# Kernel tuning notes

Measured on AMD Instinct MI355X. Metric: run time of the kernel, lower is better.

## Reference

```python
import jax, jax.numpy as jnp
import numpy as np

EPS = 1e-7

def sphere_log(p, q):
    # Riemannian log on unit sphere; p, q broadcastable, points along last axis.
    dot = jnp.clip(jnp.sum(p * q, axis=-1, keepdims=True), -1.0 + EPS, 1.0 - EPS)
    theta = jnp.arccos(dot)
    v = q - dot * p                      # tangent direction (unnormalized)
    nv = jnp.linalg.norm(v, axis=-1, keepdims=True)
    nv_safe = jnp.where(nv < EPS, 1.0, nv)
    factor = jnp.where(nv < EPS, 1.0, theta / nv_safe)  # theta/||v|| -> 1 as q->p
    return factor * v

def sphere_exp(p, v):
    # Riemannian exp on unit sphere.
    n = jnp.linalg.norm(v, axis=-1, keepdims=True)
    n_safe = jnp.where(n < EPS, 1.0, n)
    s = jnp.where(n < EPS, 1.0, jnp.sin(n_safe) / n_safe)  # sinc(||v||)
    return jnp.cos(n) * p + s * v

def setup_inputs() -> dict:
    key = jax.random.key(0)
    k1, k2 = jax.random.split(key)
    B, L, C_in, C_out, d = 4, 256, 64, 64, 64
    x = jax.random.normal(k1, (B, L, C_in, d), dtype=jnp.float32)
    x = x / jnp.linalg.norm(x, axis=-1, keepdims=True)  # points on S^{d-1}
    # param 'w': truncated_normal(stddev=1) with shape (n_in, n_out)
    w_raw = jax.random.truncated_normal(k2, -2.0, 2.0, (C_in, C_out), dtype=jnp.float32)
    return {"x": x, "w_raw": w_raw}

def reference(x, w_raw):
    B, L, C_in, d = x.shape
    C_out = w_raw.shape[1]
    # softmax-like positive, column-normalized weights
    w = jnp.exp(w_raw - np.log(C_in).astype(np.float32))
    w = w / w.sum(axis=0)[None]          # (C_in, C_out)

    xr = x.reshape(B * L, C_in, d)       # (N, C_in, d)
    # init at first in-channel point, broadcast over out channels: (N, C_out, d)
    a = jnp.broadcast_to(xr[:, 0][:, None, :], (B * L, C_out, d))

    # 3-step fixed-point iteration toward weighted Frechet mean (scan unroll=3)
    for _ in range(3):
        logs = sphere_log(a[:, :, None, :], xr[:, None, :, :])  # (N, C_out, C_in, d)
        grad = jnp.einsum('io,noid->nod', w, logs)              # (N, C_out, d)
        a = sphere_exp(a, grad)

    return a.reshape(B, L, C_out, d)
```

## Files before the change

### kernel.cpp

```cpp
#include <hip/hip_runtime.h>

#define EPSF 1e-7f
#define TS2 72

typedef __bf16 bf16;
typedef __attribute__((ext_vector_type(8))) __bf16 bf16x8;
typedef __attribute__((ext_vector_type(4))) __bf16 bf16x4;
typedef __attribute__((ext_vector_type(4))) float f32x4;
typedef __attribute__((ext_vector_type(2))) float f32x2;

__device__ __forceinline__ float quad_sum(float v) {
  v += __shfl_xor(v, 16, 64);
  v += __shfl_xor(v, 32, 64);
  return v;
}

__global__ __launch_bounds__(256, 4) void mfd_fc_mfma(
    const float* __restrict__ x, const float* __restrict__ wraw,
    float* __restrict__ out) {
  __shared__ __align__(16) bf16 Xrow[64 * TS2];
  __shared__ __align__(16) bf16 Xt[64 * TS2];
  __shared__ __align__(16) bf16 AC[64 * TS2];

  const int n = blockIdx.x;
  const int tid = threadIdx.x;
  const int wv = tid >> 6;
  const int lane = tid & 63;
  const int ln15 = lane & 15;
  const int quad = lane >> 4;
  const int q4 = 4 * quad;
  const int olane = 16 * wv + ln15;
  const float* xn = x + (size_t)n * 4096;

  const f32x2 ONE2 = {1.0f, 1.0f};
  const f32x2 PC3 = {-0.0187292994f, -0.0187292994f};
  const f32x2 PC2 = {0.0742610070f, 0.0742610070f};
  const f32x2 PC1 = {-0.2121144013f, -0.2121144013f};
  const f32x2 PC0 = {1.5707288f, 1.5707288f};
  const f32x2 PI2 = {3.14159265358979f, 3.14159265358979f};

#pragma unroll
  for (int t = 0; t < 4; ++t) {
    int idx = tid + t * 256;
    int i = idx >> 4;
    int c4 = (idx & 15) << 2;
    float4 v = reinterpret_cast<const float4*>(xn)[idx];
    bf16x4 b;
    b[0] = (bf16)v.x; b[1] = (bf16)v.y; b[2] = (bf16)v.z; b[3] = (bf16)v.w;
    *reinterpret_cast<bf16x4*>(&Xrow[i * TS2 + c4]) = b;
  }

  f32x2 wfp[4][2];
  {
    f32x2 cs2 = {0.f, 0.f};
#pragma unroll
    for (int t = 0; t < 4; ++t)
#pragma unroll
      for (int h = 0; h < 2; ++h) {
        f32x2 e;
        e.x = __expf(wraw[(16 * t + q4 + 2 * h) * 64 + olane]);
        e.y = __expf(wraw[(16 * t + q4 + 2 * h + 1) * 64 + olane]);
        wfp[t][h] = e;
        cs2 = cs2 + e;
      }
    float inv = __builtin_amdgcn_rcpf(quad_sum(cs2.x + cs2.y));
    f32x2 inv2 = {inv, inv};
#pragma unroll
    for (int t = 0; t < 4; ++t)
#pragma unroll
      for (int h = 0; h < 2; ++h) wfp[t][h] = wfp[t][h] * inv2;
  }

  float a_reg[4][4];
#pragma unroll
  for (int t = 0; t < 4; ++t) {
    float4 v = *reinterpret_cast<const float4*>(&xn[16 * t + q4]);
    a_reg[t][0] = v.x; a_reg[t][1] = v.y; a_reg[t][2] = v.z; a_reg[t][3] = v.w;
  }

  __syncthreads();

  bf16x8 xrf[4][2];
#pragma unroll
  for (int t = 0; t < 4; ++t)
#pragma unroll
    for (int ks = 0; ks < 2; ++ks)
      xrf[t][ks] = *reinterpret_cast<const bf16x8*>(
          &Xrow[(16 * t + ln15) * TS2 + ks * 32 + quad * 8]);

  bf16x8 x0f[2];
#pragma unroll
  for (int ks = 0; ks < 2; ++ks)
    x0f[ks] = *reinterpret_cast<const bf16x8*>(&Xrow[ks * 32 + quad * 8]);

  {
    int dd = tid & 63, ih = tid >> 6;
    bf16 tmp[16];
#pragma unroll
    for (int j = 0; j < 16; ++j) tmp[j] = Xrow[(16 * ih + j) * TS2 + dd];
    *reinterpret_cast<bf16x8*>(&Xt[dd * TS2 + 16 * ih]) =
        *reinterpret_cast<bf16x8*>(&tmp[0]);
    *reinterpret_cast<bf16x8*>(&Xt[dd * TS2 + 16 * ih + 8]) =
        *reinterpret_cast<bf16x8*>(&tmp[8]);
  }

  bf16* acrow = &AC[olane * TS2];
  f32x2* a2 = reinterpret_cast<f32x2*>(&a_reg[0][0]);

#pragma unroll
  for (int it = 0; it < 3; ++it) {
    f32x4 acc[4] = {f32x4{0,0,0,0}, f32x4{0,0,0,0}, f32x4{0,0,0,0}, f32x4{0,0,0,0}};
#pragma unroll
    for (int ks = 0; ks < 2; ++ks) {
      bf16x8 bfA = (it == 0)
          ? x0f[ks]
          : *reinterpret_cast<const bf16x8*>(&acrow[ks * 32 + quad * 8]);
#pragma unroll
      for (int t = 0; t < 4; ++t)
        acc[t] = __builtin_amdgcn_mfma_f32_16x16x32_bf16(xrf[t][ks], bfA, acc[t], 0, 0, 0);
    }

#pragma unroll
    for (int t = 0; t < 4; ++t) {
      bf16x4 cpk;
#pragma unroll
      for (int h = 0; h < 2; ++h) {
        f32x2 d2;
        d2.x = __builtin_amdgcn_fmed3f(acc[t][2 * h],     -1.0f + EPSF, 1.0f - EPSF);
        d2.y = __builtin_amdgcn_fmed3f(acc[t][2 * h + 1], -1.0f + EPSF, 1.0f - EPSF);
        f32x2 nd = -d2;
        f32x2 ax; ax.x = fmaxf(d2.x, nd.x); ax.y = fmaxf(d2.y, nd.y);
        f32x2 p1 = ONE2 + ax;
        f32x2 m1 = ONE2 - ax;
        f32x2 q2, r2;
        q2.x = __builtin_amdgcn_rsqf(p1.x); q2.y = __builtin_amdgcn_rsqf(p1.y);
        r2.x = __builtin_amdgcn_rsqf(m1.x); r2.y = __builtin_amdgcn_rsqf(m1.y);
        f32x2 pa = PC3 * ax + PC2;
        pa = pa * ax + PC1;
        pa = pa * ax + PC0;
        f32x2 nb = PI2 * r2 - pa;
        f32x2 sel;
        sel.x = (d2.x < 0.f) ? nb.x : pa.x;
        sel.y = (d2.y < 0.f) ? nb.y : pa.y;
        f32x2 cf = (sel * q2) * wfp[t][h];
        cpk[2 * h]     = (bf16)cf.x;
        cpk[2 * h + 1] = (bf16)cf.y;
      }
      *reinterpret_cast<bf16x4*>(&acrow[16 * t + q4]) = cpk;
    }

    if (it == 0) __syncthreads();

    f32x4 g[4] = {f32x4{0,0,0,0}, f32x4{0,0,0,0}, f32x4{0,0,0,0}, f32x4{0,0,0,0}};
#pragma unroll
    for (int ks = 0; ks < 2; ++ks) {
      bf16x8 cf = *reinterpret_cast<const bf16x8*>(&acrow[ks * 32 + quad * 8]);
#pragma unroll
      for (int t = 0; t < 4; ++t) {
        bf16x8 xtf = *reinterpret_cast<const bf16x8*>(
            &Xt[(16 * t + ln15) * TS2 + ks * 32 + quad * 8]);
        g[t] = __builtin_amdgcn_mfma_f32_16x16x32_bf16(xtf, cf, g[t], 0, 0, 0);
      }
    }

    f32x2* g2 = reinterpret_cast<f32x2*>(&g[0]);
    f32x2 sdp = {0.f, 0.f}, ggp = {0.f, 0.f};
#pragma unroll
    for (int u = 0; u < 8; ++u) {
      sdp = a2[u] * g2[u] + sdp;
      ggp = g2[u] * g2[u] + ggp;
    }
    float sdv = quad_sum(sdp.x + sdp.y);
    float gg  = quad_sum(ggp.x + ggp.y);
    float gn2 = fmaxf(gg - sdv * sdv, 0.f);
    float nrm = __builtin_amdgcn_sqrtf(gn2);
    float rev = nrm * 0.15915494309189535f;
    float sn_ = __builtin_amdgcn_sinf(rev);
    float cn  = __builtin_amdgcn_cosf(rev);
    float sn = (nrm < EPSF) ? 1.0f : sn_ * __builtin_amdgcn_rcpf(nrm);
    float coefA = cn - sn * sdv;
    f32x2 cA2 = {coefA, coefA}, sn2 = {sn, sn};
#pragma unroll
    for (int u = 0; u < 8; ++u)
      a2[u] = cA2 * a2[u] + sn2 * g2[u];
    if (it < 2) {
#pragma unroll
      for (int t = 0; t < 4; ++t) {
        bf16x4 apk;
#pragma unroll
        for (int r = 0; r < 4; ++r) apk[r] = (bf16)a_reg[t][r];
        *reinterpret_cast<bf16x4*>(&acrow[16 * t + q4]) = apk;
      }
    }
  }

  float* outn = out + (size_t)n * 4096;
#pragma unroll
  for (int t = 0; t < 4; ++t) {
    float4 v4;
    v4.x = a_reg[t][0]; v4.y = a_reg[t][1];
    v4.z = a_reg[t][2]; v4.w = a_reg[t][3];
    *reinterpret_cast<float4*>(&outn[olane * 64 + 16 * t + q4]) = v4;
  }
}

extern "C" void kernel_launch(void* const* d_in, const int* in_sizes, int n_in,
                              void* d_out, int out_size, void* d_ws, size_t ws_size,
                              hipStream_t stream) {
  const float* x = (const float*)d_in[0];
  const float* wraw = (const float*)d_in[1];
  float* out = (float*)d_out;
  (void)d_ws; (void)ws_size;

  int N = in_sizes[0] / 4096;
  mfd_fc_mfma<<<N, 256, 0, stream>>>(x, wraw, out);
}
```

Baseline: 77.70 us.

## Process two samples per block to amortize weight setup and add ILP

Each block now handles two independent points (N/2 blocks), interleaving their MFMA chains and elementwise stages so the two samples' dependent work can overlap. The weight softmax load and normalization are computed once per two samples. LDS per block doubles and register use rises, so launch bounds drop from 4 to 2 blocks per CU, which lowers occupancy. The N/2 grid assumes N is even.

```diff
diff --git a/kernel.cpp b/kernel.cpp
--- a/kernel.cpp
+++ b/kernel.cpp
@@ -2,6 +2,7 @@
 
 #define EPSF 1e-7f
 #define TS2 72
+#define SLDS (64 * TS2)
 
 typedef __bf16 bf16;
 typedef __attribute__((ext_vector_type(8))) __bf16 bf16x8;
@@ -15,14 +16,13 @@
   return v;
 }
 
-__global__ __launch_bounds__(256, 4) void mfd_fc_mfma(
+__global__ __launch_bounds__(256, 2) void mfd_fc_mfma(
     const float* __restrict__ x, const float* __restrict__ wraw,
     float* __restrict__ out) {
-  __shared__ __align__(16) bf16 Xrow[64 * TS2];
-  __shared__ __align__(16) bf16 Xt[64 * TS2];
-  __shared__ __align__(16) bf16 AC[64 * TS2];
-
-  const int n = blockIdx.x;
+  __shared__ __align__(16) bf16 Xrow[2 * SLDS];
+  __shared__ __align__(16) bf16 Xt[2 * SLDS];
+  __shared__ __align__(16) bf16 AC[2 * SLDS];
+
   const int tid = threadIdx.x;
   const int wv = tid >> 6;
   const int lane = tid & 63;
@@ -30,7 +30,7 @@
   const int quad = lane >> 4;
   const int q4 = 4 * quad;
   const int olane = 16 * wv + ln15;
-  const float* xn = x + (size_t)n * 4096;
+  const float* xb = x + (size_t)blockIdx.x * 8192;
 
   const f32x2 ONE2 = {1.0f, 1.0f};
   const f32x2 PC3 = {-0.0187292994f, -0.0187292994f};
@@ -40,14 +40,19 @@
   const f32x2 PI2 = {3.14159265358979f, 3.14159265358979f};
 
 #pragma unroll
-  for (int t = 0; t < 4; ++t) {
-    int idx = tid + t * 256;
-    int i = idx >> 4;
-    int c4 = (idx & 15) << 2;
-    float4 v = reinterpret_cast<const float4*>(xn)[idx];
-    bf16x4 b;
-    b[0] = (bf16)v.x; b[1] = (bf16)v.y; b[2] = (bf16)v.z; b[3] = (bf16)v.w;
-    *reinterpret_cast<bf16x4*>(&Xrow[i * TS2 + c4]) = b;
+  for (int s = 0; s < 2; ++s) {
+    const float* xn = xb + s * 4096;
+    bf16* XR = Xrow + s * SLDS;
+#pragma unroll
+    for (int t = 0; t < 4; ++t) {
+      int idx = tid + t * 256;
+      int i = idx >> 4;
+      int c4 = (idx & 15) << 2;
+      float4 v = reinterpret_cast<const float4*>(xn)[idx];
+      bf16x4 b;
+      b[0] = (bf16)v.x; b[1] = (bf16)v.y; b[2] = (bf16)v.z; b[3] = (bf16)v.w;
+      *reinterpret_cast<bf16x4*>(&XR[i * TS2 + c4]) = b;
+    }
   }
 
   f32x2 wfp[4][2];
@@ -71,137 +76,168 @@
       for (int h = 0; h < 2; ++h) wfp[t][h] = wfp[t][h] * inv2;
   }
 
-  float a_reg[4][4];
-#pragma unroll
-  for (int t = 0; t < 4; ++t) {
-    float4 v = *reinterpret_cast<const float4*>(&xn[16 * t + q4]);
-    a_reg[t][0] = v.x; a_reg[t][1] = v.y; a_reg[t][2] = v.z; a_reg[t][3] = v.w;
-  }
+  float a_reg[2][4][4];
+#pragma unroll
+  for (int s = 0; s < 2; ++s)
+#pragma unroll
+    for (int t = 0; t < 4; ++t) {
+      float4 v = *reinterpret_cast<const float4*>(&xb[s * 4096 + 16 * t + q4]);
+      a_reg[s][t][0] = v.x; a_reg[s][t][1] = v.y;
+      a_reg[s][t][2] = v.z; a_reg[s][t][3] = v.w;
+    }
 
   __syncthreads();
 
-  bf16x8 xrf[4][2];
-#pragma unroll
-  for (int t = 0; t < 4; ++t)
+  bf16x8 xrf[2][4][2];
+  bf16x8 x0f[2][2];
+#pragma unroll
+  for (int s = 0; s < 2; ++s) {
+    const bf16* XR = Xrow + s * SLDS;
+#pragma unroll
+    for (int t = 0; t < 4; ++t)
+#pragma unroll
+      for (int ks = 0; ks < 2; ++ks)
+        xrf[s][t][ks] = *reinterpret_cast<const bf16x8*>(
+            &XR[(16 * t + ln15) * TS2 + ks * 32 + quad * 8]);
 #pragma unroll
     for (int ks = 0; ks < 2; ++ks)
-      xrf[t][ks] = *reinterpret_cast<const bf16x8*>(
-          &Xrow[(16 * t + ln15) * TS2 + ks * 32 + quad * 8]);
-
-  bf16x8 x0f[2];
-#pragma unroll
-  for (int ks = 0; ks < 2; ++ks)
-    x0f[ks] = *reinterpret_cast<const bf16x8*>(&Xrow[ks * 32 + quad * 8]);
-
-  {
+      x0f[s][ks] = *reinterpret_cast<const bf16x8*>(&XR[ks * 32 + quad * 8]);
+  }
+
+#pragma unroll
+  for (int s = 0; s < 2; ++s) {
+    const bf16* XR = Xrow + s * SLDS;
+    bf16* XT = Xt + s * SLDS;
     int dd = tid & 63, ih = tid >> 6;
     bf16 tmp[16];
 #pragma unroll
-    for (int j = 0; j < 16; ++j) tmp[j] = Xrow[(16 * ih + j) * TS2 + dd];
-    *reinterpret_cast<bf16x8*>(&Xt[dd * TS2 + 16 * ih]) =
+    for (int j = 0; j < 16; ++j) tmp[j] = XR[(16 * ih + j) * TS2 + dd];
+    *reinterpret_cast<bf16x8*>(&XT[dd * TS2 + 16 * ih]) =
         *reinterpret_cast<bf16x8*>(&tmp[0]);
-    *reinterpret_cast<bf16x8*>(&Xt[dd * TS2 + 16 * ih + 8]) =
+    *reinterpret_cast<bf16x8*>(&XT[dd * TS2 + 16 * ih + 8]) =
         *reinterpret_cast<bf16x8*>(&tmp[8]);
   }
 
-  bf16* acrow = &AC[olane * TS2];
-  f32x2* a2 = reinterpret_cast<f32x2*>(&a_reg[0][0]);
-
 #pragma unroll
   for (int it = 0; it < 3; ++it) {
-    f32x4 acc[4] = {f32x4{0,0,0,0}, f32x4{0,0,0,0}, f32x4{0,0,0,0}, f32x4{0,0,0,0}};
-#pragma unroll
-    for (int ks = 0; ks < 2; ++ks) {
-      bf16x8 bfA = (it == 0)
-          ? x0f[ks]
-          : *reinterpret_cast<const bf16x8*>(&acrow[ks * 32 + quad * 8]);
-#pragma unroll
-      for (int t = 0; t < 4; ++t)
-        acc[t] = __builtin_amdgcn_mfma_f32_16x16x32_bf16(xrf[t][ks], bfA, acc[t], 0, 0, 0);
-    }
-
+    f32x4 acc[2][4];
+#pragma unroll
+    for (int s = 0; s < 2; ++s) {
+      const bf16* acs = AC + s * SLDS + olane * TS2;
+#pragma unroll
+      for (int t = 0; t < 4; ++t) acc[s][t] = f32x4{0, 0, 0, 0};
+#pragma unroll
+      for (int ks = 0; ks < 2; ++ks) {
+        bf16x8 bfA = (it == 0)
+            ? x0f[s][ks]
+            : *reinterpret_cast<const bf16x8*>(&acs[ks * 32 + quad * 8]);
+#pragma unroll
+        for (int t = 0; t < 4; ++t)
+          acc[s][t] = __builtin_amdgcn_mfma_f32_16x16x32_bf16(
+              xrf[s][t][ks], bfA, acc[s][t], 0, 0, 0);
+      }
+    }
+
+#pragma unroll
+    for (int s = 0; s < 2; ++s) {
+      bf16* acs = AC + s * SLDS + olane * TS2;
+#pragma unroll
+      for (int t = 0; t < 4; ++t) {
+        bf16x4 cpk;
+#pragma unroll
+        for (int h = 0; h < 2; ++h) {
+          f32x2 d2;
+          d2.x = __builtin_amdgcn_fmed3f(acc[s][t][2 * h],     -1.0f + EPSF, 1.0f - EPSF);
+          d2.y = __builtin_amdgcn_fmed3f(acc[s][t][2 * h + 1], -1.0f + EPSF, 1.0f - EPSF);
+          f32x2 nd = -d2;
+          f32x2 ax; ax.x = fmaxf(d2.x, nd.x); ax.y = fmaxf(d2.y, nd.y);
+          f32x2 p1 = ONE2 + ax;
+          f32x2 m1 = ONE2 - ax;
+          f32x2 q2, r2;
+          q2.x = __builtin_amdgcn_rsqf(p1.x); q2.y = __builtin_amdgcn_rsqf(p1.y);
+          r2.x = __builtin_amdgcn_rsqf(m1.x); r2.y = __builtin_amdgcn_rsqf(m1.y);
+          f32x2 pa = PC3 * ax + PC2;
+          pa = pa * ax + PC1;
+          pa = pa * ax + PC0;
+          f32x2 nb = PI2 * r2 - pa;
+          f32x2 sel;
+          sel.x = (d2.x < 0.f) ? nb.x : pa.x;
+          sel.y = (d2.y < 0.f) ? nb.y : pa.y;
+          f32x2 cf = (sel * q2) * wfp[t][h];
+          cpk[2 * h]     = (bf16)cf.x;
+          cpk[2 * h + 1] = (bf16)cf.y;
+        }
+        *reinterpret_cast<bf16x4*>(&acs[16 * t + q4]) = cpk;
+      }
+    }
+
+    if (it == 0) __syncthreads();
+
+    f32x4 g[2][4];
+#pragma unroll
+    for (int s = 0; s < 2; ++s) {
+      const bf16* acs = AC + s * SLDS + olane * TS2;
+      const bf16* XT = Xt + s * SLDS;
+#pragma unroll
+      for (int t = 0; t < 4; ++t) g[s][t] = f32x4{0, 0, 0, 0};
+#pragma unroll
+      for (int ks = 0; ks < 2; ++ks) {
+        bf16x8 cf = *reinterpret_cast<const bf16x8*>(&acs[ks * 32 + quad * 8]);
+#pragma unroll
+        for (int t = 0; t < 4; ++t) {
+          bf16x8 xtf = *reinterpret_cast<const bf16x8*>(
+              &XT[(16 * t + ln15) * TS2 + ks * 32 + quad * 8]);
+          g[s][t] = __builtin_amdgcn_mfma_f32_16x16x32_bf16(xtf, cf, g[s][t], 0, 0, 0);
+        }
+      }
+    }
+
+#pragma unroll
+    for (int s = 0; s < 2; ++s) {
+      f32x2* g2 = reinterpret_cast<f32x2*>(&g[s][0]);
+      f32x2* a2 = reinterpret_cast<f32x2*>(&a_reg[s][0][0]);
+      f32x2 sdp = {0.f, 0.f}, ggp = {0.f, 0.f};
+#pragma unroll
+      for (int u = 0; u < 8; ++u) {
+        sdp = a2[u] * g2[u] + sdp;
+        ggp = g2[u] * g2[u] + ggp;
+      }
+      float sdv = quad_sum(sdp.x + sdp.y);
+      float gg  = quad_sum(ggp.x + ggp.y);
+      float gn2 = fmaxf(gg - sdv * sdv, 0.f);
+      float nrm = __builtin_amdgcn_sqrtf(gn2);
+      float rev = nrm * 0.15915494309189535f;
+      float sn_ = __builtin_amdgcn_sinf(rev);
+      float cn  = __builtin_amdgcn_cosf(rev);
+      float sn = (nrm < EPSF) ? 1.0f : sn_ * __builtin_amdgcn_rcpf(nrm);
+      float coefA = cn - sn * sdv;
+      f32x2 cA2 = {coefA, coefA}, sn2 = {sn, sn};
+#pragma unroll
+      for (int u = 0; u < 8; ++u)
+        a2[u] = cA2 * a2[u] + sn2 * g2[u];
+      if (it < 2) {
+        bf16* acs = AC + s * SLDS + olane * TS2;
+#pragma unroll
+        for (int t = 0; t < 4; ++t) {
+          bf16x4 apk;
+#pragma unroll
+          for (int r = 0; r < 4; ++r) apk[r] = (bf16)a_reg[s][t][r];
+          *reinterpret_cast<bf16x4*>(&acs[16 * t + q4]) = apk;
+        }
+      }
+    }
+  }
+
+  float* outb = out + (size_t)blockIdx.x * 8192;
+#pragma unroll
+  for (int s = 0; s < 2; ++s)
 #pragma unroll
     for (int t = 0; t < 4; ++t) {
-      bf16x4 cpk;
-#pragma unroll
-      for (int h = 0; h < 2; ++h) {
-        f32x2 d2;
-        d2.x = __builtin_amdgcn_fmed3f(acc[t][2 * h],     -1.0f + EPSF, 1.0f - EPSF);
-        d2.y = __builtin_amdgcn_fmed3f(acc[t][2 * h + 1], -1.0f + EPSF, 1.0f - EPSF);
-        f32x2 nd = -d2;
-        f32x2 ax; ax.x = fmaxf(d2.x, nd.x); ax.y = fmaxf(d2.y, nd.y);
-        f32x2 p1 = ONE2 + ax;
-        f32x2 m1 = ONE2 - ax;
-        f32x2 q2, r2;
-        q2.x = __builtin_amdgcn_rsqf(p1.x); q2.y = __builtin_amdgcn_rsqf(p1.y);
-        r2.x = __builtin_amdgcn_rsqf(m1.x); r2.y = __builtin_amdgcn_rsqf(m1.y);
-        f32x2 pa = PC3 * ax + PC2;
-        pa = pa * ax + PC1;
-        pa = pa * ax + PC0;
-        f32x2 nb = PI2 * r2 - pa;
-        f32x2 sel;
-        sel.x = (d2.x < 0.f) ? nb.x : pa.x;
-        sel.y = (d2.y < 0.f) ? nb.y : pa.y;
-        f32x2 cf = (sel * q2) * wfp[t][h];
-        cpk[2 * h]     = (bf16)cf.x;
-        cpk[2 * h + 1] = (bf16)cf.y;
-      }
-      *reinterpret_cast<bf16x4*>(&acrow[16 * t + q4]) = cpk;
-    }
-
-    if (it == 0) __syncthreads();
-
-    f32x4 g[4] = {f32x4{0,0,0,0}, f32x4{0,0,0,0}, f32x4{0,0,0,0}, f32x4{0,0,0,0}};
-#pragma unroll
-    for (int ks = 0; ks < 2; ++ks) {
-      bf16x8 cf = *reinterpret_cast<const bf16x8*>(&acrow[ks * 32 + quad * 8]);
-#pragma unroll
-      for (int t = 0; t < 4; ++t) {
-        bf16x8 xtf = *reinterpret_cast<const bf16x8*>(
-            &Xt[(16 * t + ln15) * TS2 + ks * 32 + quad * 8]);
-        g[t] = __builtin_amdgcn_mfma_f32_16x16x32_bf16(xtf, cf, g[t], 0, 0, 0);
-      }
-    }
-
-    f32x2* g2 = reinterpret_cast<f32x2*>(&g[0]);
-    f32x2 sdp = {0.f, 0.f}, ggp = {0.f, 0.f};
-#pragma unroll
-    for (int u = 0; u < 8; ++u) {
-      sdp = a2[u] * g2[u] + sdp;
-      ggp = g2[u] * g2[u] + ggp;
-    }
-    float sdv = quad_sum(sdp.x + sdp.y);
-    float gg  = quad_sum(ggp.x + ggp.y);
-    float gn2 = fmaxf(gg - sdv * sdv, 0.f);
-    float nrm = __builtin_amdgcn_sqrtf(gn2);
-    float rev = nrm * 0.15915494309189535f;
-    float sn_ = __builtin_amdgcn_sinf(rev);
-    float cn  = __builtin_amdgcn_cosf(rev);
-    float sn = (nrm < EPSF) ? 1.0f : sn_ * __builtin_amdgcn_rcpf(nrm);
-    float coefA = cn - sn * sdv;
-    f32x2 cA2 = {coefA, coefA}, sn2 = {sn, sn};
-#pragma unroll
-    for (int u = 0; u < 8; ++u)
-      a2[u] = cA2 * a2[u] + sn2 * g2[u];
-    if (it < 2) {
-#pragma unroll
-      for (int t = 0; t < 4; ++t) {
-        bf16x4 apk;
-#pragma unroll
-        for (int r = 0; r < 4; ++r) apk[r] = (bf16)a_reg[t][r];
-        *reinterpret_cast<bf16x4*>(&acrow[16 * t + q4]) = apk;
-      }
-    }
-  }
-
-  float* outn = out + (size_t)n * 4096;
-#pragma unroll
-  for (int t = 0; t < 4; ++t) {
-    float4 v4;
-    v4.x = a_reg[t][0]; v4.y = a_reg[t][1];
-    v4.z = a_reg[t][2]; v4.w = a_reg[t][3];
-    *reinterpret_cast<float4*>(&outn[olane * 64 + 16 * t + q4]) = v4;
-  }
+      float4 v4;
+      v4.x = a_reg[s][t][0]; v4.y = a_reg[s][t][1];
+      v4.z = a_reg[s][t][2]; v4.w = a_reg[s][t][3];
+      *reinterpret_cast<float4*>(&outb[s * 4096 + olane * 64 + 16 * t + q4]) = v4;
+    }
 }
 
 extern "C" void kernel_launch(void* const* d_in, const int* in_sizes, int n_in,
@@ -213,5 +249,5 @@
   (void)d_ws; (void)ws_size;
 
   int N = in_sizes[0] / 4096;
-  mfd_fc_mfma<<<N, 256, 0, stream>>>(x, wraw, out);
+  mfd_fc_mfma<<<N / 2, 256, 0, stream>>>(x, wraw, out);
 }
```

Result: slower. 80.50 us (+3.6%).
